# Performance work log

Measured on AMD Instinct MI355X. Metric: run time of the kernel, lower is better.

## Reference

```python
import jax, jax.numpy as jnp
import numpy as np

EPS = 1e-5
ALPHA = 0.7
N_HEADS = 20
N_KV_HEADS = 5
HEAD_DIM = 128


def bitlinear(x, w):
    # absmean ternary quantization per output row: w_t = sign(w)*(|w| > alpha*absmean)
    absw = jnp.abs(w)
    absmean = jnp.mean(absw, axis=1, keepdims=True)            # [out, 1]
    tern = jnp.sign(w) * (absw > ALPHA * absmean).astype(w.dtype)
    # (X @ pos^T - X @ neg^T) * scale == (X @ tern^T) * scale
    return jnp.einsum('...i,oi->...o', x, tern) * absmean[:, 0]


def rmsnorm(x, g):
    var = jnp.mean(jnp.square(x), axis=-1, keepdims=True)
    return x * jax.lax.rsqrt(var + EPS) * g


def rotate_half(x):
    x1, x2 = jnp.split(x, 2, axis=-1)
    return jnp.concatenate([-x2, x1], axis=-1)


def setup_inputs() -> dict:
    key = jax.random.key(0)
    ks = jax.random.split(key, 12)
    h, inter = 2560, 6912
    b, s = 1, 2048
    wscale = 1.0 / np.sqrt(h)
    return {
        'x': jax.random.normal(ks[0], (b, s, h), jnp.float32),
        'cos': jax.random.uniform(ks[1], (1, 1, s, HEAD_DIM), jnp.float32),
        'sin': jax.random.uniform(ks[2], (1, 1, s, HEAD_DIM), jnp.float32),
        'q_w': jax.random.normal(ks[3], (h, h), jnp.float32) * wscale,
        'k_w': jax.random.normal(ks[4], (N_KV_HEADS * HEAD_DIM, h), jnp.float32) * wscale,
        'v_w': jax.random.normal(ks[5], (N_KV_HEADS * HEAD_DIM, h), jnp.float32) * wscale,
        'o_w': jax.random.normal(ks[6], (h, h), jnp.float32) * wscale,
        'gate_w': jax.random.normal(ks[7], (inter, h), jnp.float32) * wscale,
        'up_w': jax.random.normal(ks[8], (inter, h), jnp.float32) * wscale,
        'down_w': jax.random.normal(ks[9], (h, inter), jnp.float32) / np.sqrt(inter),
        'ln1_w': jnp.ones((h,), jnp.float32),
        'ln2_w': jnp.ones((h,), jnp.float32),
    }


def reference(x, cos, sin, q_w, k_w, v_w, o_w, gate_w, up_w, down_w, ln1_w, ln2_w):
    b, s, hdim = x.shape
    residual = x
    h = rmsnorm(x, ln1_w)

    q = bitlinear(h, q_w).reshape(b, s, N_HEADS, HEAD_DIM).transpose(0, 2, 1, 3)
    k = bitlinear(h, k_w).reshape(b, s, N_KV_HEADS, HEAD_DIM).transpose(0, 2, 1, 3)
    v = bitlinear(h, v_w).reshape(b, s, N_KV_HEADS, HEAD_DIM).transpose(0, 2, 1, 3)

    # RoPE
    q = q * cos + rotate_half(q) * sin
    k = k * cos + rotate_half(k) * sin

    # GQA: repeat_interleave kv heads
    n_rep = N_HEADS // N_KV_HEADS
    k = jnp.repeat(k, n_rep, axis=1)
    v = jnp.repeat(v, n_rep, axis=1)

    scale = 1.0 / np.sqrt(HEAD_DIM)
    attn = jnp.einsum('bhqd,bhkd->bhqk', q, k) * scale
    attn = jax.nn.softmax(attn, axis=-1)
    o = jnp.einsum('bhqk,bhkd->bhqd', attn, v)
    o = o.transpose(0, 2, 1, 3).reshape(b, s, hdim)

    x = residual + bitlinear(o, o_w)

    residual = x
    h = rmsnorm(x, ln2_w)
    gate = jnp.square(jax.nn.relu(bitlinear(h, gate_w)))  # relu^2
    x = residual + bitlinear(gate * bitlinear(h, up_w), down_w)
    return x
```

## Files before the change

### kernel.cpp

```cpp
#include <hip/hip_runtime.h>
#include <hip/hip_bf16.h>

typedef unsigned short u16;
typedef short bf16x8 __attribute__((ext_vector_type(8)));
typedef float f32x4 __attribute__((ext_vector_type(4)));

__device__ __forceinline__ u16 f2b(float f) {
    union { __hip_bfloat16 h; u16 u; } cv;
    cv.h = __float2bfloat16(f);
    return cv.u;
}
__device__ __forceinline__ float b2f(u16 u) {
    union { u16 u; __hip_bfloat16 h; } cv;
    cv.u = u;
    return __bfloat162float(cv.h);
}

__device__ __forceinline__ void g2l16(const void* g, void* l) {
    __builtin_amdgcn_global_load_lds(
        (const __attribute__((address_space(1))) unsigned int*)g,
        (__attribute__((address_space(3))) unsigned int*)l, 16, 0, 0);
}

template <int EPT>
__global__ __launch_bounds__(256) void quant_kernel(const float* __restrict__ W,
                                                    u16* __restrict__ T,
                                                    float* __restrict__ scales, int K) {
    const int row = blockIdx.x, tid = threadIdx.x;
    const float* wr = W + (size_t)row * K;
    float v[EPT];
    float s = 0.f;
#pragma unroll
    for (int i = 0; i < EPT; ++i) { v[i] = wr[tid + i * 256]; s += fabsf(v[i]); }
#pragma unroll
    for (int d = 1; d < 64; d <<= 1) s += __shfl_xor(s, d);
    __shared__ float red[4];
    if ((tid & 63) == 0) red[tid >> 6] = s;
    __syncthreads();
    const float absmean = (red[0] + red[1] + red[2] + red[3]) / (float)K;
    const float thr = 0.7f * absmean;
    u16* tr = T + (size_t)row * K;
#pragma unroll
    for (int i = 0; i < EPT; ++i) {
        float w = v[i];
        float t = (fabsf(w) > thr) ? ((w > 0.f) ? 1.f : -1.f) : 0.f;
        tr[tid + i * 256] = f2b(t);
    }
    if (tid == 0) scales[row] = absmean;
}

__global__ __launch_bounds__(256) void rmsnorm_kernel(const float* __restrict__ x,
                                                      const float* __restrict__ g,
                                                      u16* __restrict__ o) {
    const int row = blockIdx.x, tid = threadIdx.x;
    const float* xr = x + (size_t)row * 2560;
    float v[10];
    float s = 0.f;
#pragma unroll
    for (int i = 0; i < 10; ++i) { v[i] = xr[tid + i * 256]; s += v[i] * v[i]; }
#pragma unroll
    for (int d = 1; d < 64; d <<= 1) s += __shfl_xor(s, d);
    __shared__ float red[4];
    if ((tid & 63) == 0) red[tid >> 6] = s;
    __syncthreads();
    const float total = red[0] + red[1] + red[2] + red[3];
    const float rs = rsqrtf(total * (1.f / 2560.f) + 1e-5f);
    u16* orow = o + (size_t)row * 2560;
#pragma unroll
    for (int i = 0; i < 10; ++i) orow[tid + i * 256] = f2b(v[i] * rs * g[tid + i * 256]);
}

template <int MODE>
__global__ __launch_bounds__(256) void gemm_bt(const u16* __restrict__ A,
                                               const u16* __restrict__ B,
                                               const float* __restrict__ scale,
                                               const float* __restrict__ res,
                                               void* __restrict__ outp,
                                               int M, int N, int K) {
    __shared__ __align__(16) u16 sA[128 * 64];
    __shared__ __align__(16) u16 sB[128 * 64];
    const int tid = threadIdx.x;
    const int wave = tid >> 6, lane = tid & 63;
    const int lane15 = lane & 15, quad = lane >> 4;
    const int m0 = blockIdx.x * 128, n0 = blockIdx.y * 128;
    const int wm = wave >> 1, wn = wave & 1;

    f32x4 acc[4][4] = {};

    const int r0 = wave * 8 + (lane >> 3);
    const int gcc = (lane & 7) ^ (lane >> 3);
    const size_t aoff = (size_t)(m0 + r0) * K + gcc * 8;
    const size_t boff = (size_t)(n0 + r0) * K + gcc * 8;
    char* ldsA = (char*)sA + wave * 1024;
    char* ldsB = (char*)sB + wave * 1024;
    const int sw = lane15 & 7;

    for (int kt = 0; kt < K; kt += 64) {
#pragma unroll
        for (int s = 0; s < 4; ++s) {
            g2l16(A + aoff + (size_t)s * 32 * K + kt, ldsA + s * 4096);
            g2l16(B + boff + (size_t)s * 32 * K + kt, ldsB + s * 4096);
        }
        __syncthreads();
#pragma unroll
        for (int kc = 0; kc < 2; ++kc) {
            bf16x8 af[4], bfr[4];
            const int pc = ((kc * 4 + quad) ^ sw) * 8;
#pragma unroll
            for (int f = 0; f < 4; ++f)
                af[f] = *(const bf16x8*)&sA[(wm * 64 + f * 16 + lane15) * 64 + pc];
#pragma unroll
            for (int f = 0; f < 4; ++f)
                bfr[f] = *(const bf16x8*)&sB[(wn * 64 + f * 16 + lane15) * 64 + pc];
#pragma unroll
            for (int i = 0; i < 4; ++i)
#pragma unroll
                for (int j = 0; j < 4; ++j)
                    acc[i][j] = __builtin_amdgcn_mfma_f32_16x16x32_bf16(af[i], bfr[j], acc[i][j], 0, 0, 0);
        }
        __syncthreads();
    }

#pragma unroll
    for (int j = 0; j < 4; ++j) {
        const int c = n0 + wn * 64 + j * 16 + lane15;
        const float sc = scale[c];
#pragma unroll
        for (int i = 0; i < 4; ++i) {
            const int rbase = m0 + wm * 64 + i * 16 + quad * 4;
#pragma unroll
            for (int r = 0; r < 4; ++r) {
                const float vv = acc[i][j][r] * sc;
                const size_t idx = (size_t)(rbase + r) * N + c;
                if (MODE == 0) ((u16*)outp)[idx] = f2b(vv);
                else           ((float*)outp)[idx] = res[idx] + vv;
            }
        }
    }
}

__global__ __launch_bounds__(256) void rope_kernel(u16* __restrict__ buf,
                                                   const float* __restrict__ cs,
                                                   const float* __restrict__ sn, int nh) {
    const int idx = blockIdx.x * 256 + threadIdx.x;
    const int d = idx & 63;
    const int h = (idx >> 6) % nh;
    const int s = idx / (64 * nh);
    const size_t base = (size_t)s * (nh * 128) + h * 128;
    const float a = b2f(buf[base + d]), b = b2f(buf[base + d + 64]);
    const float c1 = cs[s * 128 + d], s1 = sn[s * 128 + d];
    const float c2 = cs[s * 128 + d + 64], s2 = sn[s * 128 + d + 64];
    buf[base + d] = f2b(a * c1 - b * s1);
    buf[base + d + 64] = f2b(b * c2 + a * s2);
}

__global__ __launch_bounds__(256) void transpose_v_kernel(const u16* __restrict__ V,
                                                          u16* __restrict__ VT) {
    __shared__ u16 t[128 * 66];
    const int tid = threadIdx.x;
    const int h = blockIdx.y, s0 = blockIdx.x * 64;
#pragma unroll
    for (int i = 0; i < 32; ++i) {
        const int idx = tid + i * 256;
        const int r = idx >> 7, c = idx & 127;
        t[c * 66 + r] = V[(size_t)(s0 + r) * 640 + h * 128 + c];
    }
    __syncthreads();
#pragma unroll
    for (int i = 0; i < 32; ++i) {
        const int idx = tid + i * 256;
        const int d = idx >> 6, s = idx & 63;
        VT[((size_t)h * 128 + d) * 2048 + s0 + s] = t[d * 66 + s];
    }
}

__global__ __launch_bounds__(256, 3) void flash_kernel(const u16* __restrict__ Q,
                                                       const u16* __restrict__ Kb,
                                                       const u16* __restrict__ VT,
                                                       u16* __restrict__ O) {
    __shared__ __align__(16) u16 sQ[64 * 128];
    __shared__ __align__(16) u16 sK[64 * 128];
    __shared__ __align__(16) u16 sV[128 * 64];
    const int tid = threadIdx.x, wave = tid >> 6, lane = tid & 63;
    const int lane15 = lane & 15, quad = lane >> 4;
    const int head = blockIdx.y, q0 = blockIdx.x * 64, kvh = head >> 2;
    const int sw = lane15 & 7;

    {
        const int rq = wave * 4 + (lane >> 4);
        const int gq = (lane & 15) ^ (rq & 7);
        const u16* src = Q + (size_t)(q0 + rq) * 2560 + head * 128 + gq * 8;
        char* dst = (char*)sQ + wave * 1024;
#pragma unroll
        for (int s = 0; s < 4; ++s)
            g2l16(src + (size_t)s * 16 * 2560, dst + s * 4096);
    }
    __syncthreads();
    bf16x8 qf[4];
#pragma unroll
    for (int kc = 0; kc < 4; ++kc)
        qf[kc] = *(const bf16x8*)&sQ[(wave * 16 + lane15) * 128 + ((kc * 4 + quad) ^ sw) * 8];

    float m_i[4], l_i[4];
    f32x4 o_acc[8] = {};
#pragma unroll
    for (int r = 0; r < 4; ++r) { m_i[r] = -1e30f; l_i[r] = 0.f; }

    const float sl2e = 0.088388347648318447f * 1.4426950408889634f;

    const int rk = wave * 4 + (lane >> 4);
    const int gk = (lane & 15) ^ (rk & 7);
    const u16* kbase = Kb + (size_t)rk * 640 + kvh * 128 + gk * 8;
    const int rv = wave * 8 + (lane >> 3);
    const int gv = (lane & 7) ^ (rv & 7);
    const u16* vbase = VT + ((size_t)kvh * 128 + rv) * 2048 + gv * 8;
    char* dstK = (char*)sK + wave * 1024;
    char* dstV = (char*)sV + wave * 1024;
    u16* sP = sQ;

    for (int k0 = 0; k0 < 2048; k0 += 64) {
#pragma unroll
        for (int s = 0; s < 4; ++s) {
            g2l16(kbase + ((size_t)k0 + s * 16) * 640, dstK + s * 4096);
            g2l16(vbase + (size_t)s * 32 * 2048 + k0, dstV + s * 4096);
        }
        __syncthreads();

        f32x4 sacc[4] = {};
#pragma unroll
        for (int nf = 0; nf < 4; ++nf)
#pragma unroll
            for (int kc = 0; kc < 4; ++kc) {
                const bf16x8 kf = *(const bf16x8*)&sK[(nf * 16 + lane15) * 128 + ((kc * 4 + quad) ^ sw) * 8];
                sacc[nf] = __builtin_amdgcn_mfma_f32_16x16x32_bf16(qf[kc], kf, sacc[nf], 0, 0, 0);
            }

#pragma unroll
        for (int r = 0; r < 4; ++r) {
            float v0 = sacc[0][r] * sl2e, v1 = sacc[1][r] * sl2e;
            float v2 = sacc[2][r] * sl2e, v3 = sacc[3][r] * sl2e;
            float mx = fmaxf(fmaxf(v0, v1), fmaxf(v2, v3));
#pragma unroll
            for (int d = 1; d < 16; d <<= 1) mx = fmaxf(mx, __shfl_xor(mx, d));
            const float mnew = fmaxf(m_i[r], mx);
            const float alpha = exp2f(m_i[r] - mnew);
            m_i[r] = mnew;
            const float p0 = exp2f(v0 - mnew), p1 = exp2f(v1 - mnew);
            const float p2 = exp2f(v2 - mnew), p3 = exp2f(v3 - mnew);
            sacc[0][r] = p0; sacc[1][r] = p1; sacc[2][r] = p2; sacc[3][r] = p3;
            float sum = (p0 + p1) + (p2 + p3);
#pragma unroll
            for (int d = 1; d < 16; d <<= 1) sum += __shfl_xor(sum, d);
            l_i[r] = l_i[r] * alpha + sum;
#pragma unroll
            for (int nf = 0; nf < 8; ++nf) o_acc[nf][r] *= alpha;
        }

#pragma unroll
        for (int nf = 0; nf < 4; ++nf) {
            const int cc = nf * 2 + (lane15 >> 3);
            const int pcol = ((cc ^ quad) * 8) + (lane15 & 7);
#pragma unroll
            for (int r = 0; r < 4; ++r)
                sP[(wave * 16 + quad * 4 + r) * 64 + pcol] = f2b(sacc[nf][r]);
        }

        bf16x8 pf[2];
#pragma unroll
        for (int kc = 0; kc < 2; ++kc)
            pf[kc] = *(const bf16x8*)&sP[(wave * 16 + lane15) * 64 + ((kc * 4 + quad) ^ ((lane15 >> 2) & 3)) * 8];
#pragma unroll
        for (int nf = 0; nf < 8; ++nf)
#pragma unroll
            for (int kc = 0; kc < 2; ++kc) {
                const bf16x8 vf = *(const bf16x8*)&sV[(nf * 16 + lane15) * 64 + ((kc * 4 + quad) ^ sw) * 8];
                o_acc[nf] = __builtin_amdgcn_mfma_f32_16x16x32_bf16(pf[kc], vf, o_acc[nf], 0, 0, 0);
            }
        __syncthreads();
    }

#pragma unroll
    for (int r = 0; r < 4; ++r) {
        const float inv = 1.f / l_i[r];
        const int row = q0 + wave * 16 + quad * 4 + r;
        u16* orow = O + (size_t)row * 2560 + head * 128;
#pragma unroll
        for (int nf = 0; nf < 8; ++nf)
            orow[nf * 16 + lane15] = f2b(o_acc[nf][r] * inv);
    }
}

__global__ __launch_bounds__(256) void glu_kernel(u16* __restrict__ g, const u16* __restrict__ u) {
    const size_t i = ((size_t)blockIdx.x * 256 + threadIdx.x) * 8;
    bf16x8 gv = *(const bf16x8*)(g + i);
    bf16x8 uv = *(const bf16x8*)(u + i);
    bf16x8 ov;
#pragma unroll
    for (int j = 0; j < 8; ++j) {
        float x = b2f((u16)gv[j]);
        x = fmaxf(x, 0.f);
        ov[j] = (short)f2b(x * x * b2f((u16)uv[j]));
    }
    *(bf16x8*)(g + i) = ov;
}

extern "C" void kernel_launch(void* const* d_in, const int* in_sizes, int n_in,
                              void* d_out, int out_size, void* d_ws, size_t ws_size,
                              hipStream_t stream) {
    (void)in_sizes; (void)n_in; (void)out_size; (void)ws_size;
    const float* x      = (const float*)d_in[0];
    const float* cosb   = (const float*)d_in[1];
    const float* sinb   = (const float*)d_in[2];
    const float* q_w    = (const float*)d_in[3];
    const float* k_w    = (const float*)d_in[4];
    const float* v_w    = (const float*)d_in[5];
    const float* o_w    = (const float*)d_in[6];
    const float* gate_w = (const float*)d_in[7];
    const float* up_w   = (const float*)d_in[8];
    const float* down_w = (const float*)d_in[9];
    const float* ln1    = (const float*)d_in[10];
    const float* ln2    = (const float*)d_in[11];

    char* w = (char*)d_ws;
    size_t off = 0;
    auto nxt = [&](size_t sz) { char* p = w + off; off += sz; return p; };
    u16*   TQ = (u16*)nxt(13107200);
    u16*   TK = (u16*)nxt(3276800);
    u16*   TV = (u16*)nxt(3276800);
    u16*   TO = (u16*)nxt(13107200);
    u16*   TB = (u16*)nxt(35389440);
    float* SC = (float*)nxt(91136);
    u16*   H  = (u16*)nxt(10485760);
    u16*   QB = (u16*)nxt(10485760);
    u16*   KB = (u16*)nxt(2621440);
    u16*   VB = (u16*)nxt(2621440);
    u16*   VT = (u16*)nxt(2621440);
    float* XM = (float*)nxt(20971520);
    u16*   G  = (u16*)nxt(28311552);
    u16*   U  = TQ;

    quant_kernel<10><<<2560, 256, 0, stream>>>(q_w, TQ, SC + 0, 2560);
    quant_kernel<10><<<640, 256, 0, stream>>>(k_w, TK, SC + 2560, 2560);
    quant_kernel<10><<<640, 256, 0, stream>>>(v_w, TV, SC + 3200, 2560);
    quant_kernel<10><<<2560, 256, 0, stream>>>(o_w, TO, SC + 3840, 2560);
    rmsnorm_kernel<<<2048, 256, 0, stream>>>(x, ln1, H);
    gemm_bt<0><<<dim3(16, 20), 256, 0, stream>>>(H, TQ, SC + 0, nullptr, QB, 2048, 2560, 2560);
    gemm_bt<0><<<dim3(16, 5), 256, 0, stream>>>(H, TK, SC + 2560, nullptr, KB, 2048, 640, 2560);
    gemm_bt<0><<<dim3(16, 5), 256, 0, stream>>>(H, TV, SC + 3200, nullptr, VB, 2048, 640, 2560);
    rope_kernel<<<10240, 256, 0, stream>>>(QB, cosb, sinb, 20);
    rope_kernel<<<2560, 256, 0, stream>>>(KB, cosb, sinb, 5);
    transpose_v_kernel<<<dim3(32, 5), 256, 0, stream>>>(VB, VT);
    flash_kernel<<<dim3(32, 20), 256, 0, stream>>>(QB, KB, VT, H);
    gemm_bt<1><<<dim3(16, 20), 256, 0, stream>>>(H, TO, SC + 3840, x, XM, 2048, 2560, 2560);

    rmsnorm_kernel<<<2048, 256, 0, stream>>>(XM, ln2, H);
    quant_kernel<10><<<6912, 256, 0, stream>>>(gate_w, TB, SC + 6400, 2560);
    gemm_bt<0><<<dim3(16, 54), 256, 0, stream>>>(H, TB, SC + 6400, nullptr, G, 2048, 6912, 2560);
    quant_kernel<10><<<6912, 256, 0, stream>>>(up_w, TB, SC + 13312, 2560);
    gemm_bt<0><<<dim3(16, 54), 256, 0, stream>>>(H, TB, SC + 13312, nullptr, U, 2048, 6912, 2560);
    glu_kernel<<<6912, 256, 0, stream>>>(G, U);
    quant_kernel<27><<<2560, 256, 0, stream>>>(down_w, TB, SC + 20224, 6912);
    gemm_bt<1><<<dim3(16, 20), 256, 0, stream>>>(G, TB, SC + 20224, XM, (float*)d_out, 2048, 2560, 6912);
}
```

Measured before the change: 1.003 ms.

## Fuse QKV projections into one GEMM and use 8-wave GEMM blocks

```diff
diff --git a/kernel.cpp b/kernel.cpp
--- a/kernel.cpp
+++ b/kernel.cpp
@@ -71,21 +71,21 @@
 }
 
 template <int MODE>
-__global__ __launch_bounds__(256) void gemm_bt(const u16* __restrict__ A,
-                                               const u16* __restrict__ B,
-                                               const float* __restrict__ scale,
-                                               const float* __restrict__ res,
-                                               void* __restrict__ outp,
-                                               int M, int N, int K) {
+__global__ __launch_bounds__(512, 4) void gemm_bt(const u16* __restrict__ A,
+                                                  const u16* __restrict__ B,
+                                                  const float* __restrict__ scale,
+                                                  const float* __restrict__ res,
+                                                  void* __restrict__ outp,
+                                                  int M, int N, int K) {
     __shared__ __align__(16) u16 sA[128 * 64];
     __shared__ __align__(16) u16 sB[128 * 64];
     const int tid = threadIdx.x;
     const int wave = tid >> 6, lane = tid & 63;
     const int lane15 = lane & 15, quad = lane >> 4;
     const int m0 = blockIdx.x * 128, n0 = blockIdx.y * 128;
-    const int wm = wave >> 1, wn = wave & 1;
-
-    f32x4 acc[4][4] = {};
+    const int wm = wave >> 2, wn = wave & 3;
+
+    f32x4 acc[4][2] = {};
 
     const int r0 = wave * 8 + (lane >> 3);
     const int gcc = (lane & 7) ^ (lane >> 3);
@@ -96,34 +96,33 @@
     const int sw = lane15 & 7;
 
     for (int kt = 0; kt < K; kt += 64) {
-#pragma unroll
-        for (int s = 0; s < 4; ++s) {
-            g2l16(A + aoff + (size_t)s * 32 * K + kt, ldsA + s * 4096);
-            g2l16(B + boff + (size_t)s * 32 * K + kt, ldsB + s * 4096);
-        }
+        g2l16(A + aoff + kt, ldsA);
+        g2l16(A + aoff + (size_t)64 * K + kt, ldsA + 8192);
+        g2l16(B + boff + kt, ldsB);
+        g2l16(B + boff + (size_t)64 * K + kt, ldsB + 8192);
         __syncthreads();
 #pragma unroll
         for (int kc = 0; kc < 2; ++kc) {
-            bf16x8 af[4], bfr[4];
             const int pc = ((kc * 4 + quad) ^ sw) * 8;
+            bf16x8 af[4], bfr[2];
 #pragma unroll
             for (int f = 0; f < 4; ++f)
                 af[f] = *(const bf16x8*)&sA[(wm * 64 + f * 16 + lane15) * 64 + pc];
 #pragma unroll
-            for (int f = 0; f < 4; ++f)
-                bfr[f] = *(const bf16x8*)&sB[(wn * 64 + f * 16 + lane15) * 64 + pc];
+            for (int f = 0; f < 2; ++f)
+                bfr[f] = *(const bf16x8*)&sB[(wn * 32 + f * 16 + lane15) * 64 + pc];
 #pragma unroll
             for (int i = 0; i < 4; ++i)
 #pragma unroll
-                for (int j = 0; j < 4; ++j)
+                for (int j = 0; j < 2; ++j)
                     acc[i][j] = __builtin_amdgcn_mfma_f32_16x16x32_bf16(af[i], bfr[j], acc[i][j], 0, 0, 0);
         }
         __syncthreads();
     }
 
 #pragma unroll
-    for (int j = 0; j < 4; ++j) {
-        const int c = n0 + wn * 64 + j * 16 + lane15;
+    for (int j = 0; j < 2; ++j) {
+        const int c = n0 + wn * 32 + j * 16 + lane15;
         const float sc = scale[c];
 #pragma unroll
         for (int i = 0; i < 4; ++i) {
@@ -139,14 +138,14 @@
     }
 }
 
-__global__ __launch_bounds__(256) void rope_kernel(u16* __restrict__ buf,
+__global__ __launch_bounds__(256) void rope_kernel(u16* __restrict__ buf, int stride,
                                                    const float* __restrict__ cs,
                                                    const float* __restrict__ sn, int nh) {
     const int idx = blockIdx.x * 256 + threadIdx.x;
     const int d = idx & 63;
     const int h = (idx >> 6) % nh;
     const int s = idx / (64 * nh);
-    const size_t base = (size_t)s * (nh * 128) + h * 128;
+    const size_t base = (size_t)s * stride + h * 128;
     const float a = b2f(buf[base + d]), b = b2f(buf[base + d + 64]);
     const float c1 = cs[s * 128 + d], s1 = sn[s * 128 + d];
     const float c2 = cs[s * 128 + d + 64], s2 = sn[s * 128 + d + 64];
@@ -154,7 +153,7 @@
     buf[base + d + 64] = f2b(b * c2 + a * s2);
 }
 
-__global__ __launch_bounds__(256) void transpose_v_kernel(const u16* __restrict__ V,
+__global__ __launch_bounds__(256) void transpose_v_kernel(const u16* __restrict__ V, int stride,
                                                           u16* __restrict__ VT) {
     __shared__ u16 t[128 * 66];
     const int tid = threadIdx.x;
@@ -163,7 +162,7 @@
     for (int i = 0; i < 32; ++i) {
         const int idx = tid + i * 256;
         const int r = idx >> 7, c = idx & 127;
-        t[c * 66 + r] = V[(size_t)(s0 + r) * 640 + h * 128 + c];
+        t[c * 66 + r] = V[(size_t)(s0 + r) * stride + h * 128 + c];
     }
     __syncthreads();
 #pragma unroll
@@ -174,7 +173,7 @@
     }
 }
 
-__global__ __launch_bounds__(256, 3) void flash_kernel(const u16* __restrict__ Q,
+__global__ __launch_bounds__(256, 3) void flash_kernel(const u16* __restrict__ Q, int qs,
                                                        const u16* __restrict__ Kb,
                                                        const u16* __restrict__ VT,
                                                        u16* __restrict__ O) {
@@ -189,11 +188,11 @@
     {
         const int rq = wave * 4 + (lane >> 4);
         const int gq = (lane & 15) ^ (rq & 7);
-        const u16* src = Q + (size_t)(q0 + rq) * 2560 + head * 128 + gq * 8;
+        const u16* src = Q + (size_t)(q0 + rq) * qs + head * 128 + gq * 8;
         char* dst = (char*)sQ + wave * 1024;
 #pragma unroll
         for (int s = 0; s < 4; ++s)
-            g2l16(src + (size_t)s * 16 * 2560, dst + s * 4096);
+            g2l16(src + (size_t)s * 16 * qs, dst + s * 4096);
     }
     __syncthreads();
     bf16x8 qf[4];
@@ -210,7 +209,7 @@
 
     const int rk = wave * 4 + (lane >> 4);
     const int gk = (lane & 15) ^ (rk & 7);
-    const u16* kbase = Kb + (size_t)rk * 640 + kvh * 128 + gk * 8;
+    const u16* kbase = Kb + (size_t)rk * qs + kvh * 128 + gk * 8;
     const int rv = wave * 8 + (lane >> 3);
     const int gv = (lane & 7) ^ (rv & 7);
     const u16* vbase = VT + ((size_t)kvh * 128 + rv) * 2048 + gv * 8;
@@ -221,7 +220,7 @@
     for (int k0 = 0; k0 < 2048; k0 += 64) {
 #pragma unroll
         for (int s = 0; s < 4; ++s) {
-            g2l16(kbase + ((size_t)k0 + s * 16) * 640, dstK + s * 4096);
+            g2l16(kbase + ((size_t)k0 + s * 16) * qs, dstK + s * 4096);
             g2l16(vbase + (size_t)s * 32 * 2048 + k0, dstV + s * 4096);
         }
         __syncthreads();
@@ -331,9 +330,7 @@
     u16*   TB = (u16*)nxt(35389440);
     float* SC = (float*)nxt(91136);
     u16*   H  = (u16*)nxt(10485760);
-    u16*   QB = (u16*)nxt(10485760);
-    u16*   KB = (u16*)nxt(2621440);
-    u16*   VB = (u16*)nxt(2621440);
+    u16*   QKV = (u16*)nxt(15728640);
     u16*   VT = (u16*)nxt(2621440);
     float* XM = (float*)nxt(20971520);
     u16*   G  = (u16*)nxt(28311552);
@@ -344,21 +341,19 @@
     quant_kernel<10><<<640, 256, 0, stream>>>(v_w, TV, SC + 3200, 2560);
     quant_kernel<10><<<2560, 256, 0, stream>>>(o_w, TO, SC + 3840, 2560);
     rmsnorm_kernel<<<2048, 256, 0, stream>>>(x, ln1, H);
-    gemm_bt<0><<<dim3(16, 20), 256, 0, stream>>>(H, TQ, SC + 0, nullptr, QB, 2048, 2560, 2560);
-    gemm_bt<0><<<dim3(16, 5), 256, 0, stream>>>(H, TK, SC + 2560, nullptr, KB, 2048, 640, 2560);
-    gemm_bt<0><<<dim3(16, 5), 256, 0, stream>>>(H, TV, SC + 3200, nullptr, VB, 2048, 640, 2560);
-    rope_kernel<<<10240, 256, 0, stream>>>(QB, cosb, sinb, 20);
-    rope_kernel<<<2560, 256, 0, stream>>>(KB, cosb, sinb, 5);
-    transpose_v_kernel<<<dim3(32, 5), 256, 0, stream>>>(VB, VT);
-    flash_kernel<<<dim3(32, 20), 256, 0, stream>>>(QB, KB, VT, H);
-    gemm_bt<1><<<dim3(16, 20), 256, 0, stream>>>(H, TO, SC + 3840, x, XM, 2048, 2560, 2560);
+    gemm_bt<0><<<dim3(16, 30), 512, 0, stream>>>(H, TQ, SC + 0, nullptr, QKV, 2048, 3840, 2560);
+    rope_kernel<<<10240, 256, 0, stream>>>(QKV, 3840, cosb, sinb, 20);
+    rope_kernel<<<2560, 256, 0, stream>>>(QKV + 2560, 3840, cosb, sinb, 5);
+    transpose_v_kernel<<<dim3(32, 5), 256, 0, stream>>>(QKV + 3200, 3840, VT);
+    flash_kernel<<<dim3(32, 20), 256, 0, stream>>>(QKV, 3840, QKV + 2560, VT, H);
+    gemm_bt<1><<<dim3(16, 20), 512, 0, stream>>>(H, TO, SC + 3840, x, XM, 2048, 2560, 2560);
 
     rmsnorm_kernel<<<2048, 256, 0, stream>>>(XM, ln2, H);
     quant_kernel<10><<<6912, 256, 0, stream>>>(gate_w, TB, SC + 6400, 2560);
-    gemm_bt<0><<<dim3(16, 54), 256, 0, stream>>>(H, TB, SC + 6400, nullptr, G, 2048, 6912, 2560);
+    gemm_bt<0><<<dim3(16, 54), 512, 0, stream>>>(H, TB, SC + 6400, nullptr, G, 2048, 6912, 2560);
     quant_kernel<10><<<6912, 256, 0, stream>>>(up_w, TB, SC + 13312, 2560);
-    gemm_bt<0><<<dim3(16, 54), 256, 0, stream>>>(H, TB, SC + 13312, nullptr, U, 2048, 6912, 2560);
+    gemm_bt<0><<<dim3(16, 54), 512, 0, stream>>>(H, TB, SC + 13312, nullptr, U, 2048, 6912, 2560);
     glu_kernel<<<6912, 256, 0, stream>>>(G, U);
     quant_kernel<27><<<2560, 256, 0, stream>>>(down_w, TB, SC + 20224, 6912);
-    gemm_bt<1><<<dim3(16, 20), 256, 0, stream>>>(G, TB, SC + 20224, XM, (float*)d_out, 2048, 2560, 6912);
-}
+    gemm_bt<1><<<dim3(16, 20), 512, 0, stream>>>(G, TB, SC + 20224, XM, (float*)d_out, 2048, 2560, 6912);
+}
```

Result: faster. 852.2 us (-15.1%).
